# Optimization experiments

Hardware: AMD Instinct MI355X
Metric: run time of the kernel (lower is better)

## Reference

```python
import jax, jax.numpy as jnp
import numpy as np
import math

B, T, D, H = 2, 2048, 1024, 16
DH = D // H          # 64
NB = DH // 2         # 32 rotary pairs
EPS = 1e-5


def setup_inputs() -> dict:
    key = jax.random.key(0)
    ks = jax.random.split(key, 20)
    x = jax.random.normal(ks[0], (B, T, D), dtype=jnp.float32)
    angles = jax.random.uniform(ks[1], (B, H, T, NB), dtype=jnp.float32) * (2.0 * math.pi)
    cos_a = jnp.cos(angles)
    sin_a = jnp.sin(angles)
    sigma = jax.random.uniform(ks[2], (B, T, H, NB), dtype=jnp.float32)
    causal_mask = jnp.triu(jnp.ones((T, T), dtype=bool), k=1)  # True above diag -> masked
    w = lambda k, i, o: jax.random.normal(k, (i, o), dtype=jnp.float32) * 0.02
    return {
        "x": x, "cos_a": cos_a, "sin_a": sin_a, "sigma": sigma, "causal_mask": causal_mask,
        "ln1_g": jnp.ones((D,), jnp.float32), "ln1_b": jnp.zeros((D,), jnp.float32),
        "wq": w(ks[3], D, D), "bq": jnp.zeros((D,), jnp.float32),
        "wk": w(ks[4], D, D), "bk": jnp.zeros((D,), jnp.float32),
        "wv": w(ks[5], D, D), "bv": jnp.zeros((D,), jnp.float32),
        "wo": w(ks[6], D, D), "bo": jnp.zeros((D,), jnp.float32),
        "ln2_g": jnp.ones((D,), jnp.float32), "ln2_b": jnp.zeros((D,), jnp.float32),
        "w1": w(ks[7], D, 4 * D), "b1": jnp.zeros((4 * D,), jnp.float32),
        "w2": w(ks[8], 4 * D, D), "b2": jnp.zeros((D,), jnp.float32),
    }


def _layer_norm(x, g, b):
    mu = jnp.mean(x, axis=-1, keepdims=True)
    var = jnp.mean(jnp.square(x - mu), axis=-1, keepdims=True)
    return (x - mu) * jax.lax.rsqrt(var + EPS) * g + b


def _apply_rope(q, cos_a, sin_a):
    # q: (B,H,T,DH); rotate even/odd pairs by per-pair angles (B,H,T,NB)
    q1 = q[..., 0::2]
    q2 = q[..., 1::2]
    re = q1 * cos_a - q2 * sin_a
    im = q1 * sin_a + q2 * cos_a
    return jnp.stack([re, im], axis=-1).reshape(q.shape)


def reference(x, cos_a, sin_a, sigma, causal_mask,
              ln1_g, ln1_b, wq, bq, wk, bk, wv, bv, wo, bo,
              ln2_g, ln2_b, w1, b1, w2, b2):
    h = _layer_norm(x, ln1_g, ln1_b)
    Q = (h @ wq + bq).reshape(B, T, H, DH).transpose(0, 2, 1, 3)
    K = (h @ wk + bk).reshape(B, T, H, DH).transpose(0, 2, 1, 3)
    V = (h @ wv + bv).reshape(B, T, H, DH).transpose(0, 2, 1, 3)
    Q = _apply_rope(Q, cos_a, sin_a)
    K = _apply_rope(K, cos_a, sin_a)
    # per-(B,H,T) temperature from mean uncertainty
    temp = 1.0 + jnp.mean(sigma, axis=-1).transpose(0, 2, 1)  # (B,H,T)
    scale = math.sqrt(DH)
    scores = jnp.einsum("bhtd,bhsd->bhts", Q, K) / (scale * temp[..., None])
    scores = jnp.where(causal_mask[None, None], -jnp.inf, scores)
    attn = jax.nn.softmax(scores, axis=-1)
    out = jnp.einsum("bhts,bhsd->bhtd", attn, V)
    out = out.transpose(0, 2, 1, 3).reshape(B, T, D)
    x = x + (out @ wo + bo)
    h2 = _layer_norm(x, ln2_g, ln2_b)
    ffn = jax.nn.gelu(h2 @ w1 + b1, approximate=False) @ w2 + b2
    return x + ffn
```

## Files before the change

kernel.cpp:

```cpp
#include <hip/hip_runtime.h>

typedef unsigned short ushort;
typedef unsigned int uint;

typedef __attribute__((ext_vector_type(8))) short short8;
typedef __attribute__((ext_vector_type(8))) unsigned short ushort8;
typedef __attribute__((ext_vector_type(4))) unsigned short ushort4v;
typedef __attribute__((ext_vector_type(4))) float f32x4;
typedef __attribute__((ext_vector_type(4))) uint uint4v;

#define DEV static __device__ __forceinline__

DEV ushort f2b(float f){
  union { float f; uint u; } v; v.f = f;
  uint u = v.u;
  u += 0x7fffu + ((u >> 16) & 1u);
  return (ushort)(u >> 16);
}
DEV float b2f(ushort h){
  union { uint u; float f; } v; v.u = ((uint)h) << 16;
  return v.f;
}
DEV uint cvt_pk_bf16(float lo, float hi){
  uint r;
  asm("v_cvt_pk_bf16_f32 %0, %1, %2" : "=v"(r) : "v"(lo), "v"(hi));
  return r;
}
DEV ushort f2b1(float f){ return (ushort)cvt_pk_bf16(f, f); }
DEV float exp2v(float x){
  float r;
  asm("v_exp_f32 %0, %1" : "=v"(r) : "v"(x));
  return r;
}
DEV float gelu_f(float x){
  float z = fabsf(x) * 0.70710678118654752f;
  float t = __builtin_amdgcn_rcpf(1.f + 0.3275911f * z);
  float poly = t * (0.254829592f + t * (-0.284496736f + t * (1.421413741f +
               t * (-1.453152027f + t * 1.061405429f))));
  float e = exp2v(-z * z * 1.44269504088896f);
  float erf_abs = 1.f - poly * e;
  float erf_s = copysignf(erf_abs, x);
  return 0.5f * x * (1.f + erf_s);
}

constexpr int Bc = 2, Tc = 2048, Dc = 1024, Hc = 16, DHc = 64, NBc = 32;
constexpr int Rc = Bc * Tc;
constexpr int D4c = 4 * Dc;

__global__ __launch_bounds__(256) void k_transcvt_all(
    const float* __restrict__ wq, const float* __restrict__ wk, const float* __restrict__ wv,
    const float* __restrict__ wo, const float* __restrict__ w1, const float* __restrict__ w2,
    ushort* __restrict__ wqT, ushort* __restrict__ wkT, ushort* __restrict__ wvT,
    ushort* __restrict__ woT, ushort* __restrict__ w1T, ushort* __restrict__ w2T){
  __shared__ float tile[32][33];
  const int bid = blockIdx.x;
  const float* in; ushort* out; int K, N, bx, by;
  if (bid < 4096){
    int seg = bid >> 10, loc = bid & 1023;
    in  = seg == 0 ? wq  : seg == 1 ? wk  : seg == 2 ? wv  : wo;
    out = seg == 0 ? wqT : seg == 1 ? wkT : seg == 2 ? wvT : woT;
    K = 1024; N = 1024; bx = loc & 31; by = loc >> 5;
  } else if (bid < 8192){
    int loc = bid - 4096;
    in = w1; out = w1T; K = 1024; N = 4096; bx = loc & 127; by = loc >> 7;
  } else {
    int loc = bid - 8192;
    in = w2; out = w2T; K = 4096; N = 1024; bx = loc & 31; by = loc >> 5;
  }
  int n0 = bx * 32, k0 = by * 32;
  int c = threadIdx.x & 31, r0 = threadIdx.x >> 5;
#pragma unroll
  for (int i = 0; i < 4; i++){
    int k = r0 + i * 8;
    tile[k][c] = in[(size_t)(k0 + k) * N + n0 + c];
  }
  __syncthreads();
#pragma unroll
  for (int i = 0; i < 4; i++){
    int n = r0 + i * 8;
    out[(size_t)(n0 + n) * K + k0 + c] = f2b(tile[c][n]);
  }
}

__global__ __launch_bounds__(256) void k_ln(const float* __restrict__ x, const float* __restrict__ g,
                                            const float* __restrict__ bb, ushort* __restrict__ out){
  int row = blockIdx.x, tid = threadIdx.x;
  const f32x4* xr = (const f32x4*)(x + (size_t)row * Dc);
  f32x4 v = xr[tid];
  float s  = v.x + v.y + v.z + v.w;
  float ss = v.x*v.x + v.y*v.y + v.z*v.z + v.w*v.w;
#pragma unroll
  for (int off = 32; off > 0; off >>= 1){
    s  += __shfl_xor(s,  off, 64);
    ss += __shfl_xor(ss, off, 64);
  }
  __shared__ float red[2][4];
  int w = tid >> 6;
  if ((tid & 63) == 0){ red[0][w] = s; red[1][w] = ss; }
  __syncthreads();
  s  = red[0][0] + red[0][1] + red[0][2] + red[0][3];
  ss = red[1][0] + red[1][1] + red[1][2] + red[1][3];
  float mu  = s * (1.f / Dc);
  float var = ss * (1.f / Dc) - mu * mu;
  float rs  = rsqrtf(var + 1e-5f);
  f32x4 gv = ((const f32x4*)g)[tid];
  f32x4 bv = ((const f32x4*)bb)[tid];
  ushort4v o;
  o.x = f2b((v.x - mu) * rs * gv.x + bv.x);
  o.y = f2b((v.y - mu) * rs * gv.y + bv.y);
  o.z = f2b((v.z - mu) * rs * gv.z + bv.z);
  o.w = f2b((v.w - mu) * rs * gv.w + bv.w);
  ((ushort4v*)(out + (size_t)row * Dc))[tid] = o;
}

#define GLDS(src, dst) __builtin_amdgcn_global_load_lds( \
    (const __attribute__((address_space(1))) void*)(src), \
    (__attribute__((address_space(3))) void*)(dst), 16, 0, 0)

#define STAGE64(nb_, k0_) do { \
  _Pragma("unroll") \
  for (int i_ = 0; i_ < 4; i_++){ \
    int chunk_ = w * 4 + i_; \
    GLDS(A + (size_t)(m0 + chunk_ * 8 + rloc) * K + (k0_) + gsrc * 8, &SM[nb_][chunk_ * 512]); \
  } \
  _Pragma("unroll") \
  for (int j_ = 0; j_ < 2; j_++){ \
    int chunk_ = w * 2 + j_; \
    GLDS(Bt + (size_t)(n0 + chunk_ * 8 + rloc) * K + (k0_) + gsrc * 8, &SM[nb_][8192 + chunk_ * 512]); \
  } \
} while(0)

#define CORE64(cb_) do { \
  _Pragma("unroll") \
  for (int ks = 0; ks < 2; ks++){ \
    const int gs = (ks * 4 + lg) ^ l7; \
    short8 aF[2], bF[4]; \
    _Pragma("unroll") \
    for (int mi = 0; mi < 2; mi++) aF[mi] = *(const short8*)&SM[cb_][(arow + mi * 16) * 64 + gs * 8]; \
    _Pragma("unroll") \
    for (int ni = 0; ni < 4; ni++) bF[ni] = *(const short8*)&SM[cb_][8192 + (ni * 16 + la15) * 64 + gs * 8]; \
    _Pragma("unroll") \
    for (int mi = 0; mi < 2; mi++) \
      _Pragma("unroll") \
      for (int ni = 0; ni < 4; ni++) \
        acc[mi][ni] = __builtin_amdgcn_mfma_f32_16x16x32_bf16(aF[mi], bF[ni], acc[mi][ni], 0, 0, 0); \
  } \
} while(0)

#define N64_LOOP() do { \
  STAGE64(0, 0); \
  __syncthreads(); \
  const int NT_ = K >> 6; \
  for (int t = 0; t < NT_; t++){ \
    const int cb = t & 1; \
    if (t + 1 < NT_) STAGE64(cb ^ 1, (t + 1) << 6); \
    CORE64(cb); \
    __syncthreads(); \
  } \
} while(0)

__global__ __launch_bounds__(256) void k_gemm_n64(const ushort* __restrict__ A, const ushort* __restrict__ Bt,
                                                  const float* __restrict__ bias, const float* __restrict__ resid,
                                                  float* __restrict__ Cout, int M, int N, int K){
  __shared__ ushort SM[2][12288];
  const int tid = threadIdx.x;
  const int m0 = blockIdx.y * 128, n0 = blockIdx.x * 64;
  const int w = tid >> 6, lane = tid & 63;
  const int la15 = lane & 15, lg = lane >> 4, l7 = lane & 7;
  const int rloc = lane >> 3, gsrc = (lane & 7) ^ rloc;

  f32x4 acc[2][4];
#pragma unroll
  for (int i = 0; i < 2; i++)
#pragma unroll
    for (int j = 0; j < 4; j++) acc[i][j] = f32x4{0.f, 0.f, 0.f, 0.f};

  const int arow = w * 32 + la15;

  N64_LOOP();

#pragma unroll
  for (int mi = 0; mi < 2; mi++)
#pragma unroll
    for (int ni = 0; ni < 4; ni++){
      int cc = n0 + ni * 16 + la15;
      float bv = bias[cc];
      f32x4 a4 = acc[mi][ni];
#pragma unroll
      for (int r = 0; r < 4; r++){
        int rr = m0 + w * 32 + mi * 16 + lg * 4 + r;
        float v = a4[r] + bv + resid[(size_t)rr * N + cc];
        Cout[(size_t)rr * N + cc] = v;
      }
    }
}

__global__ __launch_bounds__(256) void k_gemm_n64b(const ushort* __restrict__ A, const ushort* __restrict__ Bt,
                                                   const float* __restrict__ bias,
                                                   ushort* __restrict__ Cout, int M, int N, int K){
  __shared__ ushort SM[2][12288];
  const int tid = threadIdx.x;
  const int m0 = blockIdx.y * 128, n0 = blockIdx.x * 64;
  const int w = tid >> 6, lane = tid & 63;
  const int la15 = lane & 15, lg = lane >> 4, l7 = lane & 7;
  const int rloc = lane >> 3, gsrc = (lane & 7) ^ rloc;

  f32x4 acc[2][4];
#pragma unroll
  for (int i = 0; i < 2; i++)
#pragma unroll
    for (int j = 0; j < 4; j++) acc[i][j] = f32x4{0.f, 0.f, 0.f, 0.f};

  const int arow = w * 32 + la15;

  N64_LOOP();

  ushort* Cs = &SM[0][0];
#pragma unroll
  for (int mi = 0; mi < 2; mi++)
#pragma unroll
    for (int ni = 0; ni < 4; ni++){
      int ccl = ni * 16 + la15;
      float bv = bias[n0 + ccl];
      f32x4 a4 = acc[mi][ni];
#pragma unroll
      for (int r = 0; r < 4; r++){
        int rl = w * 32 + mi * 16 + lg * 4 + r;
        Cs[rl * 72 + ccl] = f2b1(gelu_f(a4[r] + bv));
      }
    }
  __syncthreads();
#pragma unroll
  for (int p = 0; p < 4; p++){
    int row = p * 32 + (tid >> 3);
    int col = (tid & 7) * 8;
    ushort8 vv = *(const ushort8*)&Cs[row * 72 + col];
    *(ushort8*)(Cout + (size_t)(m0 + row) * N + n0 + col) = vv;
  }
}

__global__ __launch_bounds__(256) void k_gemm_qkv64(const ushort* __restrict__ A, const ushort* __restrict__ Bt,
                                                    const float* __restrict__ bq_, const float* __restrict__ bk_,
                                                    const float* __restrict__ bv_, ushort* __restrict__ oq,
                                                    ushort* __restrict__ ok, ushort* __restrict__ ovt,
                                                    const float* __restrict__ cosa, const float* __restrict__ sina,
                                                    int K){
  __shared__ ushort SM[2][12288];
  const int tid = threadIdx.x;
  const int m0 = blockIdx.y * 128, n0 = blockIdx.x * 64;
  const int w = tid >> 6, lane = tid & 63;
  const int la15 = lane & 15, lg = lane >> 4, l7 = lane & 7;
  const int rloc = lane >> 3, gsrc = (lane & 7) ^ rloc;

  f32x4 acc[2][4];
#pragma unroll
  for (int i = 0; i < 2; i++)
#pragma unroll
    for (int j = 0; j < 4; j++) acc[i][j] = f32x4{0.f, 0.f, 0.f, 0.f};

  const int arow = w * 32 + la15;

  N64_LOOP();

  const int sel = n0 >> 10;
  ushort* Cs = &SM[0][0];
  if (sel < 2){
    const float* bias = sel == 0 ? bq_ : bk_;
    ushort* o = sel == 0 ? oq : ok;
#pragma unroll
    for (int mi = 0; mi < 2; mi++)
#pragma unroll
      for (int ni = 0; ni < 4; ni++){
        int ccl = ni * 16 + la15;
        float bv = bias[(n0 & 1023) + ccl];
        f32x4 a4 = acc[mi][ni];
#pragma unroll
        for (int r = 0; r < 4; r++){
          int rl = w * 32 + mi * 16 + lg * 4 + r;
          Cs[rl * 72 + ccl] = f2b1(a4[r] + bv);
        }
      }
    __syncthreads();
#pragma unroll
    for (int p = 0; p < 4; p++){
      int row = p * 32 + (tid >> 3);
      int col = (tid & 7) * 8;
      ushort8 vv = *(const ushort8*)&Cs[row * 72 + col];
      int rr = m0 + row;
      int bb2 = rr >> 11, tt2 = rr & 2047;
      int cg = (n0 & 1023) + col;
      int hh2 = cg >> 6;
      int nb0 = (cg & 63) >> 1;
      size_t ai = ((size_t)(bb2 * Hc + hh2) * Tc + tt2) * NBc + nb0;
      f32x4 cv = *(const f32x4*)(cosa + ai);
      f32x4 sv = *(const f32x4*)(sina + ai);
      ushort8 ov;
#pragma unroll
      for (int j2 = 0; j2 < 4; j2++){
        float x1 = b2f((ushort)vv[2 * j2]), x2 = b2f((ushort)vv[2 * j2 + 1]);
        uint pk = cvt_pk_bf16(x1 * cv[j2] - x2 * sv[j2], x1 * sv[j2] + x2 * cv[j2]);
        ov[2 * j2]     = (ushort)(pk & 0xffff);
        ov[2 * j2 + 1] = (ushort)(pk >> 16);
      }
      *(ushort8*)(o + (size_t)rr * Dc + cg) = ov;
    }
  } else {
#pragma unroll
    for (int mi = 0; mi < 2; mi++)
#pragma unroll
      for (int ni = 0; ni < 4; ni++){
        int ccl = ni * 16 + la15;
        float bv = bv_[(n0 - 2048) + ccl];
        f32x4 a4 = acc[mi][ni];
#pragma unroll
        for (int r = 0; r < 4; r++){
          int rl = w * 32 + mi * 16 + lg * 4 + r;
          Cs[ccl * 136 + rl] = f2b1(a4[r] + bv);
        }
      }
    __syncthreads();
    const int bb = m0 >> 11, t0 = m0 & 2047;
#pragma unroll
    for (int p = 0; p < 4; p++){
      int nl = p * 16 + (tid >> 4);
      int tl = (tid & 15) * 8;
      ushort8 vv = *(const ushort8*)&Cs[nl * 136 + tl];
      int ng = (n0 - 2048) + nl;
      *(ushort8*)(ovt + ((size_t)(bb * 1024 + ng) << 11) + t0 + tl) = vv;
    }
  }
}

__global__ __launch_bounds__(256) void k_iscale(const float* __restrict__ sigma, float* __restrict__ isc){
  int idx = blockIdx.x * 256 + threadIdx.x;
  int hh = idx & 15;
  int t  = (idx >> 4) & 2047;
  int b  = idx >> 15;
  const f32x4* sp = (const f32x4*)(sigma + (size_t)idx * NBc);
  float s = 0.f;
#pragma unroll
  for (int i = 0; i < 8; i++){ f32x4 v = sp[i]; s += v.x + v.y + v.z + v.w; }
  isc[(b * Hc + hh) * Tc + t] = 1.44269504088896f / (8.f * (1.f + s * (1.f / NBc)));
}

__global__ __launch_bounds__(64) void k_attn_mfma(const ushort* __restrict__ qb, const ushort* __restrict__ kb,
                                                  const ushort* __restrict__ vtb, const float* __restrict__ isc,
                                                  ushort* __restrict__ ao){
  __shared__ ushort smem[8192];
  const int bid = blockIdx.x;
  const int bh = bid & 31, b = bh >> 4, h = bh & 15;
  const int qt = 63 - (bid >> 5);
  const int lane = threadIdx.x;
  const int la15 = lane & 15, lg = lane >> 4, l7 = lane & 7;
  const int q0w = qt * 32;

  short8 qf[2][2];
  float iscv[2];
#pragma unroll
  for (int sub = 0; sub < 2; sub++){
    int qg = q0w + sub * 16 + la15;
    size_t rb = (size_t)(b * Tc + qg) * Dc + h * DHc;
    qf[sub][0] = *(const short8*)(qb + rb + lg * 8);
    qf[sub][1] = *(const short8*)(qb + rb + 32 + lg * 8);
    iscv[sub] = isc[bh * Tc + qg];
  }

  f32x4 O[2][4];
#pragma unroll
  for (int sub = 0; sub < 2; sub++)
#pragma unroll
    for (int dt = 0; dt < 4; dt++) O[sub][dt] = f32x4{0.f, 0.f, 0.f, 0.f};
  float lacc[2] = {0.f, 0.f};

  const ushort* kbase  = kb + (size_t)b * Tc * Dc + h * DHc;
  const ushort* vtbase = vtb + (size_t)bh * DHc * Tc;
  const int ktmax = q0w + 31;

  const int Rl = lane >> 3, sl = lane & 7;
  const int gV = sl ^ (Rl & 7);

#define STAGE_KV(kt_) do { \
  _Pragma("unroll") \
  for (int i_ = 0; i_ < 8; i_++){ \
    int R_ = i_ * 8 + Rl; \
    int gk_ = sl ^ ((R_ & 3) ^ (((R_ >> 3) & 3) << 1)); \
    GLDS(kbase + (size_t)((kt_) + R_) * Dc + gk_ * 8, &smem[i_ * 512]); \
    GLDS(vtbase + (size_t)R_ * Tc + (kt_) + gV * 8, &smem[4096 + i_ * 512]); \
  } \
} while(0)

#define COMPUTE_T(kt_) do { \
  _Pragma("unroll") \
  for (int sub = 0; sub < 2; sub++){ \
    f32x4 s_[4]; \
    __builtin_amdgcn_s_setprio(1); \
    _Pragma("unroll") \
    for (int t_ = 0; t_ < 4; t_++){ \
      s_[t_] = f32x4{0.f, 0.f, 0.f, 0.f}; \
      s_[t_] = __builtin_amdgcn_mfma_f32_16x16x32_bf16(kf[t_][0], qf[sub][0], s_[t_], 0, 0, 0); \
      s_[t_] = __builtin_amdgcn_mfma_f32_16x16x32_bf16(kf[t_][1], qf[sub][1], s_[t_], 0, 0, 0); \
    } \
    __builtin_amdgcn_s_setprio(0); \
    const int qg_ = q0w + sub * 16 + la15; \
    const float sc_ = iscv[sub]; \
    const bool diag_ = ((kt_) + 63 > q0w + sub * 16); \
    uint up_[4][2]; \
    float lp_ = 0.f; \
    _Pragma("unroll") \
    for (int t_ = 0; t_ < 4; t_++){ \
      _Pragma("unroll") \
      for (int pr_ = 0; pr_ < 2; pr_++){ \
        float e0_ = exp2v(s_[t_][2 * pr_] * sc_); \
        float e1_ = exp2v(s_[t_][2 * pr_ + 1] * sc_); \
        if (diag_){ \
          int kp0_ = (kt_) + ((t_ >> 1) << 5) + lg * 8 + ((t_ & 1) << 2) + 2 * pr_; \
          if (kp0_ > qg_)     e0_ = 0.f; \
          if (kp0_ + 1 > qg_) e1_ = 0.f; \
        } \
        lp_ += e0_ + e1_; \
        up_[t_][pr_] = cvt_pk_bf16(e0_, e1_); \
      } \
    } \
    lacc[sub] += lp_; \
    __builtin_amdgcn_s_setprio(1); \
    _Pragma("unroll") \
    for (int kh_ = 0; kh_ < 2; kh_++){ \
      union { uint4v w; short8 s8; } pfr_; \
      pfr_.w[0] = up_[kh_ * 2][0];     pfr_.w[1] = up_[kh_ * 2][1]; \
      pfr_.w[2] = up_[kh_ * 2 + 1][0]; pfr_.w[3] = up_[kh_ * 2 + 1][1]; \
      _Pragma("unroll") \
      for (int dt_ = 0; dt_ < 4; dt_++) \
        O[sub][dt_] = __builtin_amdgcn_mfma_f32_16x16x32_bf16(vtf[dt_][kh_], pfr_.s8, O[sub][dt_], 0, 0, 0); \
    } \
    __builtin_amdgcn_s_setprio(0); \
  } \
} while(0)

  STAGE_KV(0);
  asm volatile("s_waitcnt vmcnt(0)" ::: "memory");
  __builtin_amdgcn_sched_barrier(0);

  for (int kt = 0;; kt += 64){
    short8 kf[4][2], vtf[4][2];
#pragma unroll
    for (int t_ = 0; t_ < 4; t_++){
      int r = ((t_ >> 1) << 5) + ((la15 >> 2) << 3) + ((t_ & 1) << 2) + (la15 & 3);
#pragma unroll
      for (int ds = 0; ds < 2; ds++){
        int g = (ds * 4 + lg) ^ ((la15 & 3) ^ ((la15 >> 2) << 1));
        kf[t_][ds] = *(const short8*)&smem[r * 64 + g * 8];
      }
    }
#pragma unroll
    for (int dt = 0; dt < 4; dt++){
      int d = dt * 16 + la15;
#pragma unroll
      for (int kh = 0; kh < 2; kh++){
        int g = (kh * 4 + lg) ^ (la15 & 7);
        vtf[dt][kh] = *(const short8*)&smem[4096 + d * 64 + g * 8];
      }
    }
    asm volatile("s_waitcnt lgkmcnt(0)" ::: "memory");
    __builtin_amdgcn_sched_barrier(0);
    STAGE_KV(kt + 64);
    COMPUTE_T(kt);
    if (kt + 64 > ktmax) break;
    asm volatile("s_waitcnt vmcnt(0)" ::: "memory");
    __builtin_amdgcn_sched_barrier(0);
  }
  asm volatile("s_waitcnt vmcnt(0)" ::: "memory");
  __builtin_amdgcn_sched_barrier(0);

  char* osb = (char*)smem;
#pragma unroll
  for (int sub = 0; sub < 2; sub++){
    float lt = lacc[sub];
    lt += __shfl_xor(lt, 16, 64);
    lt += __shfl_xor(lt, 32, 64);
    float inv = 1.f / lt;
#pragma unroll
    for (int dt = 0; dt < 4; dt++)
#pragma unroll
      for (int pr = 0; pr < 2; pr++){
        uint u = cvt_pk_bf16(O[sub][dt][2 * pr] * inv, O[sub][dt][2 * pr + 1] * inv);
        *(uint*)(osb + (sub * 16 + la15) * 136 + (dt * 16 + lg * 4 + pr * 2) * 2) = u;
      }
  }
#pragma unroll
  for (int it = 0; it < 4; it++){
    int ql = it * 8 + (lane >> 3);
    ushort8 v = *(const ushort8*)(osb + ql * 136 + l7 * 16);
    *(ushort8*)(ao + (size_t)(b * Tc + q0w + ql) * Dc + h * DHc + l7 * 8) = v;
  }
}

extern "C" void kernel_launch(void* const* d_in, const int* in_sizes, int n_in,
                              void* d_out, int out_size, void* d_ws, size_t ws_size,
                              hipStream_t stream){
  (void)in_sizes; (void)n_in; (void)out_size; (void)ws_size;
  const float* x    = (const float*)d_in[0];
  const float* cosa = (const float*)d_in[1];
  const float* sina = (const float*)d_in[2];
  const float* sigma= (const float*)d_in[3];
  const float* ln1g = (const float*)d_in[5];
  const float* ln1b = (const float*)d_in[6];
  const float* wq   = (const float*)d_in[7];
  const float* bq   = (const float*)d_in[8];
  const float* wk   = (const float*)d_in[9];
  const float* bk   = (const float*)d_in[10];
  const float* wv   = (const float*)d_in[11];
  const float* bv   = (const float*)d_in[12];
  const float* wo   = (const float*)d_in[13];
  const float* bo   = (const float*)d_in[14];
  const float* ln2g = (const float*)d_in[15];
  const float* ln2b = (const float*)d_in[16];
  const float* w1   = (const float*)d_in[17];
  const float* b1   = (const float*)d_in[18];
  const float* w2   = (const float*)d_in[19];
  const float* b2   = (const float*)d_in[20];
  float* out = (float*)d_out;

  char* ws = (char*)d_ws;
  constexpr size_t MB = 1024 * 1024;
  ushort* wqT  = (ushort*)(ws +  0 * MB);
  ushort* wkT  = (ushort*)(ws +  2 * MB);
  ushort* wvT  = (ushort*)(ws +  4 * MB);
  ushort* woT  = (ushort*)(ws +  6 * MB);
  ushort* w1T  = (ushort*)(ws +  8 * MB);
  ushort* w2T  = (ushort*)(ws + 16 * MB);
  ushort* hb   = (ushort*)(ws + 24 * MB);
  ushort* qbuf = (ushort*)(ws + 32 * MB);
  ushort* kbuf = (ushort*)(ws + 40 * MB);
  ushort* vtb  = (ushort*)(ws + 48 * MB);
  ushort* aob  = (ushort*)(ws + 56 * MB);
  float*  x2   = (float*)(ws + 64 * MB);
  float*  iscp = (float*)(ws + 80 * MB);
  ushort* g1b  = qbuf;

  k_transcvt_all<<<12288, 256, 0, stream>>>(wq, wk, wv, wo, w1, w2, wqT, wkT, wvT, woT, w1T, w2T);
  k_ln<<<Rc, 256, 0, stream>>>(x, ln1g, ln1b, hb);
  k_gemm_qkv64<<<dim3(3 * Dc / 64, Rc / 128), 256, 0, stream>>>(hb, wqT, bq, bk, bv, qbuf, kbuf, vtb,
                                                                cosa, sina, Dc);
  k_iscale<<<(Bc * Tc * Hc) / 256, 256, 0, stream>>>(sigma, iscp);
  k_attn_mfma<<<dim3(2048), 64, 0, stream>>>(qbuf, kbuf, vtb, iscp, aob);
  k_gemm_n64<<<dim3(Dc / 64, Rc / 128), 256, 0, stream>>>(aob, woT, bo, x, x2, Rc, Dc, Dc);
  k_ln<<<Rc, 256, 0, stream>>>(x2, ln2g, ln2b, hb);
  k_gemm_n64b<<<dim3(D4c / 64, Rc / 128), 256, 0, stream>>>(hb, w1T, b1, g1b, Rc, D4c, Dc);
  k_gemm_n64<<<dim3(Dc / 64, Rc / 128), 256, 0, stream>>>(g1b, w2T, b2, x2, out, Rc, Dc, D4c);
}
```

Baseline: 225.9 us.

## Share K/V tiles across two waves per attention block

The attention kernel now runs two waves per block, each owning 32 query rows of a 64-row tile. Wave 0 stages K while wave 1 stages V into shared memory, so each K/V tile is loaded once for 64 queries instead of once per 32. Per-wave direct vmcnt waits are replaced by __syncthreads barriers. The cost is block-level synchronisation, half as many blocks, and the lower wave idling on the diagonal tile.

After: 220.6 us (median of 3 runs). 2.4% less time.

```diff
diff --git a/kernel.cpp b/kernel.cpp
--- a/kernel.cpp
+++ b/kernel.cpp
@@ -343,16 +343,18 @@
   isc[(b * Hc + hh) * Tc + t] = 1.44269504088896f / (8.f * (1.f + s * (1.f / NBc)));
 }
 
-__global__ __launch_bounds__(64) void k_attn_mfma(const ushort* __restrict__ qb, const ushort* __restrict__ kb,
-                                                  const ushort* __restrict__ vtb, const float* __restrict__ isc,
-                                                  ushort* __restrict__ ao){
+__global__ __launch_bounds__(128) void k_attn_mfma(const ushort* __restrict__ qb, const ushort* __restrict__ kb,
+                                                   const ushort* __restrict__ vtb, const float* __restrict__ isc,
+                                                   ushort* __restrict__ ao){
   __shared__ ushort smem[8192];
   const int bid = blockIdx.x;
   const int bh = bid & 31, b = bh >> 4, h = bh & 15;
-  const int qt = 63 - (bid >> 5);
-  const int lane = threadIdx.x;
+  const int qt = 31 - (bid >> 5);
+  const int tid = threadIdx.x;
+  const int wq = tid >> 6, lane = tid & 63;
   const int la15 = lane & 15, lg = lane >> 4, l7 = lane & 7;
-  const int q0w = qt * 32;
+  const int q0 = qt * 64;
+  const int q0w = q0 + wq * 32;
 
   short8 qf[2][2];
   float iscv[2];
@@ -374,18 +376,24 @@
 
   const ushort* kbase  = kb + (size_t)b * Tc * Dc + h * DHc;
   const ushort* vtbase = vtb + (size_t)bh * DHc * Tc;
-  const int ktmax = q0w + 31;
 
   const int Rl = lane >> 3, sl = lane & 7;
   const int gV = sl ^ (Rl & 7);
 
 #define STAGE_KV(kt_) do { \
-  _Pragma("unroll") \
-  for (int i_ = 0; i_ < 8; i_++){ \
-    int R_ = i_ * 8 + Rl; \
-    int gk_ = sl ^ ((R_ & 3) ^ (((R_ >> 3) & 3) << 1)); \
-    GLDS(kbase + (size_t)((kt_) + R_) * Dc + gk_ * 8, &smem[i_ * 512]); \
-    GLDS(vtbase + (size_t)R_ * Tc + (kt_) + gV * 8, &smem[4096 + i_ * 512]); \
+  if (wq == 0){ \
+    _Pragma("unroll") \
+    for (int i_ = 0; i_ < 8; i_++){ \
+      int R_ = i_ * 8 + Rl; \
+      int gk_ = sl ^ ((R_ & 3) ^ (((R_ >> 3) & 3) << 1)); \
+      GLDS(kbase + (size_t)((kt_) + R_) * Dc + gk_ * 8, &smem[i_ * 512]); \
+    } \
+  } else { \
+    _Pragma("unroll") \
+    for (int i_ = 0; i_ < 8; i_++){ \
+      int R_ = i_ * 8 + Rl; \
+      GLDS(vtbase + (size_t)R_ * Tc + (kt_) + gV * 8, &smem[4096 + i_ * 512]); \
+    } \
   } \
 } while(0)
 
@@ -437,9 +445,9 @@
 } while(0)
 
   STAGE_KV(0);
-  asm volatile("s_waitcnt vmcnt(0)" ::: "memory");
-  __builtin_amdgcn_sched_barrier(0);
-
+  __syncthreads();
+
+  const int ktend = q0 + 63;
   for (int kt = 0;; kt += 64){
     short8 kf[4][2], vtf[4][2];
 #pragma unroll
@@ -462,16 +470,15 @@
     }
     asm volatile("s_waitcnt lgkmcnt(0)" ::: "memory");
     __builtin_amdgcn_sched_barrier(0);
+    __syncthreads();
     STAGE_KV(kt + 64);
-    COMPUTE_T(kt);
-    if (kt + 64 > ktmax) break;
-    asm volatile("s_waitcnt vmcnt(0)" ::: "memory");
-    __builtin_amdgcn_sched_barrier(0);
-  }
-  asm volatile("s_waitcnt vmcnt(0)" ::: "memory");
-  __builtin_amdgcn_sched_barrier(0);
-
-  char* osb = (char*)smem;
+    if (kt <= q0w + 31) COMPUTE_T(kt);
+    if (kt + 64 > ktend) break;
+    __syncthreads();
+  }
+  __syncthreads();
+
+  char* osb = (char*)smem + wq * 4352;
 #pragma unroll
   for (int sub = 0; sub < 2; sub++){
     float lt = lacc[sub];
@@ -542,7 +549,7 @@
   k_gemm_qkv64<<<dim3(3 * Dc / 64, Rc / 128), 256, 0, stream>>>(hb, wqT, bq, bk, bv, qbuf, kbuf, vtb,
                                                                 cosa, sina, Dc);
   k_iscale<<<(Bc * Tc * Hc) / 256, 256, 0, stream>>>(sigma, iscp);
-  k_attn_mfma<<<dim3(2048), 64, 0, stream>>>(qbuf, kbuf, vtb, iscp, aob);
+  k_attn_mfma<<<dim3(1024), 128, 0, stream>>>(qbuf, kbuf, vtb, iscp, aob);
   k_gemm_n64<<<dim3(Dc / 64, Rc / 128), 256, 0, stream>>>(aob, woT, bo, x, x2, Rc, Dc, Dc);
   k_ln<<<Rc, 256, 0, stream>>>(x2, ln2g, ln2b, hb);
   k_gemm_n64b<<<dim3(D4c / 64, Rc / 128), 256, 0, stream>>>(hb, w1T, b1, g1b, Rc, D4c, Dc);
```
